# Kernel optimization log

Hardware: AMD Instinct MI355X
Metric: run time of the kernel (lower is better)

The kernel has to match this reference:

```python
import jax, jax.numpy as jnp
import numpy as np
from jax import lax

B, T, D, H, L = 512, 512, 32, 64, 2
ALPHA, BETA = 2.0 / 5.0, 4.0 / 5.0  # GRUFlowBlock contraction constants


def setup_inputs() -> dict:
    key = jax.random.key(0)
    ks = jax.random.split(key, 16)
    s = 1.0 / np.sqrt(H + 1)
    inp = {
        "x": jax.random.normal(ks[0], (B, T, D), jnp.float32),
        "t": jax.random.uniform(ks[1], (B, T, 1), jnp.float32),
        # GRU-flow layer params (spectral norm folded into weight values)
        "flow_W_hr": jax.random.normal(ks[2], (L, H, H + 1), jnp.float32) * s,
        "flow_b_hr": jax.random.normal(ks[3], (L, H), jnp.float32) * 0.01,
        "flow_W_hz": jax.random.normal(ks[4], (L, H, H + 1), jnp.float32) * s,
        "flow_b_hz": jax.random.normal(ks[5], (L, H), jnp.float32) * 0.01,
        "flow_W_hh": jax.random.normal(ks[6], (L, H, H + 1), jnp.float32) * s,
        "flow_b_hh": jax.random.normal(ks[7], (L, H), jnp.float32) * 0.01,
        # TimeTanh: tanh(w * t), per-dim scale w
        "flow_tw": jax.random.normal(ks[8], (L, H), jnp.float32),
        # nn.GRU(D, H) single layer, batch_first
        "gru_W_ih": jax.random.normal(ks[9], (3 * H, D), jnp.float32) / np.sqrt(H),
        "gru_W_hh": jax.random.normal(ks[10], (3 * H, H), jnp.float32) / np.sqrt(H),
        "gru_b_ih": jax.random.normal(ks[11], (3 * H,), jnp.float32) / np.sqrt(H),
        "gru_b_hh": jax.random.normal(ks[12], (3 * H,), jnp.float32) / np.sqrt(H),
    }
    return inp


def _flow(h, tt, flow_W_hr, flow_b_hr, flow_W_hz, flow_b_hz, flow_W_hh, flow_b_hh, flow_tw):
    # h: [B, H], tt: [B, 1]
    for l in range(L):
        inp = jnp.concatenate([h, tt], -1)  # [B, H+1]
        r = BETA * jax.nn.sigmoid(inp @ flow_W_hr[l].T + flow_b_hr[l])
        z = ALPHA * jax.nn.sigmoid(inp @ flow_W_hz[l].T + flow_b_hz[l])
        u = jnp.tanh(jnp.concatenate([r * h, tt], -1) @ flow_W_hh[l].T + flow_b_hh[l])
        h = h + jnp.tanh(flow_tw[l] * tt) * (z * (u - h))
    return h


def _gru_cell(xt, h, gru_W_ih, gru_W_hh, gru_b_ih, gru_b_hh):
    gi = xt @ gru_W_ih.T + gru_b_ih  # [B, 3H]
    gh = h @ gru_W_hh.T + gru_b_hh
    i_r, i_z, i_n = jnp.split(gi, 3, -1)
    h_r, h_z, h_n = jnp.split(gh, 3, -1)
    r = jax.nn.sigmoid(i_r + h_r)
    z = jax.nn.sigmoid(i_z + h_z)
    n = jnp.tanh(i_n + r * h_n)
    return (1.0 - z) * n + z * h


def reference(x, t, flow_W_hr, flow_b_hr, flow_W_hz, flow_b_hz, flow_W_hh, flow_b_hh,
              flow_tw, gru_W_ih, gru_W_hh, gru_b_ih, gru_b_hh):
    def step(h, xt_tt):
        xt, tt = xt_tt  # [B, D], [B, 1]
        h = _flow(h, tt, flow_W_hr, flow_b_hr, flow_W_hz, flow_b_hz,
                  flow_W_hh, flow_b_hh, flow_tw)
        h_out = h  # hiddens stores the post-flow, pre-GRU state
        h_new = _gru_cell(xt, h, gru_W_ih, gru_W_hh, gru_b_ih, gru_b_hh)
        return h_new, h_out

    h0 = jnp.zeros((x.shape[0], H), x.dtype)
    xs = (jnp.swapaxes(x, 0, 1), jnp.swapaxes(t, 0, 1))  # time-major for scan
    _, hiddens = lax.scan(step, h0, xs)  # [T, B, H]
    return jnp.swapaxes(hiddens, 0, 1)  # [B, T, H]
```

## Files before the change

kernel.cpp:

```cpp
#include <hip/hip_runtime.h>


#define NT 512
#define ND 32
#define NH 64
#define NL 2

__device__ __forceinline__ float sigm(float v) {
    return __builtin_amdgcn_rcpf(1.0f + __expf(-v));
}
__device__ __forceinline__ float tanh_(float v) {
    return 1.0f - 2.0f * __builtin_amdgcn_rcpf(1.0f + __expf(2.0f * v));
}

__global__ __launch_bounds__(512, 4) void cgru_fused(
    const float* __restrict__ x, const float* __restrict__ tin,
    const float* __restrict__ Whr, const float* __restrict__ bhr,
    const float* __restrict__ Whz, const float* __restrict__ bhz,
    const float* __restrict__ Whh, const float* __restrict__ bhh,
    const float* __restrict__ tw,
    const float* __restrict__ gWih, const float* __restrict__ gWhh,
    const float* __restrict__ gbih, const float* __restrict__ gbhh,
    float* __restrict__ out)
{
    const int tid = threadIdx.x;
    const int j   = tid >> 3;
    const int q   = tid & 7;
    const int qh  = q & 3;
    const bool isZ = q >= 4;
    const int b   = blockIdx.x;

    __shared__ float hS[NH];
    __shared__ float rhS[NH];
    __shared__ float hxS[128];

    const float* Wsrc = isZ ? Whz : Whr;
    const float* bsrc = isZ ? bhz : bhr;
    float wrz[NL][16], wu[NL][8];
    float w65rz[NL], w65u[NL], brz[NL], bu[NL], tws[NL];
#pragma unroll
    for (int l = 0; l < NL; ++l) {
        const int row = (l * NH + j) * (NH + 1);
#pragma unroll
        for (int k = 0; k < 16; ++k) wrz[l][k] = Wsrc[row + qh * 16 + k];
#pragma unroll
        for (int k = 0; k < 8; ++k)  wu[l][k]  = Whh[row + q * 8 + k];
        w65rz[l] = Wsrc[row + NH];
        w65u[l]  = Whh[row + NH];
        brz[l]   = bsrc[l * NH + j];
        bu[l]    = bhh[l * NH + j];
        tws[l]   = tw[l * NH + j];
    }

    const int grow = (isZ ? NH : 0) + j;
    float g1[24];
#pragma unroll
    for (int k = 0; k < 24; ++k) {
        const int m = qh * 24 + k;
        g1[k] = (m < NH) ? gWhh[grow * NH + m] : gWih[grow * ND + (m - NH)];
    }
    const float bg1 = gbih[grow] + gbhh[grow];

    float g2[16];
    if (!isZ) {
#pragma unroll
        for (int k = 0; k < 16; ++k) g2[k] = gWhh[(2 * NH + j) * NH + qh * 16 + k];
    } else {
#pragma unroll
        for (int k = 0; k < 8; ++k)  g2[k] = gWih[(2 * NH + j) * ND + qh * 8 + k];
#pragma unroll
        for (int k = 8; k < 16; ++k) g2[k] = 0.0f;
    }
    const float bin = gbih[2 * NH + j];
    const float bhn = gbhh[2 * NH + j];

    if (tid < NH) hS[tid] = 0.0f;
    if (tid < 32) hxS[96 + tid] = 0.0f;
    __syncthreads();

    const float* xp = x + (size_t)b * NT * ND;
    const float* tp = tin + (size_t)b * NT;
    float* op = out + (size_t)b * NT * NH;

    for (int ts = 0; ts < NT; ++ts) {
        const float tt = tp[ts];
        float xv = 0.0f;
        if (tid < ND) xv = xp[ts * ND + tid];

#pragma unroll
        for (int l = 0; l < NL; ++l) {
            float a = 0.0f;
            {
                const float* hp = &hS[qh * 16];
#pragma unroll
                for (int k = 0; k < 16; ++k) a = fmaf(wrz[l][k], hp[k], a);
            }
            a += __shfl_xor(a, 1);
            a += __shfl_xor(a, 2);
            const float s  = sigm(a + w65rz[l] * tt + brz[l]);
            const float zv = 0.4f * s;
            if (q == 0) rhS[j] = (0.8f * s) * hS[j];
            __syncthreads();

            float u = 0.0f;
            {
                const float* rp = &rhS[q * 8];
#pragma unroll
                for (int k = 0; k < 8; ++k) u = fmaf(wu[l][k], rp[k], u);
            }
            u += __shfl_xor(u, 1);
            u += __shfl_xor(u, 2);
            u += __shfl_xor(u, 4);
            if (l == NL - 1 && tid < ND) hxS[NH + tid] = xv;
            const float uu = tanh_(u + w65u[l] * tt + bu[l]);
            if (q == 4) {
                const float hj = hS[j];
                const float hn = fmaf(tanh_(tws[l] * tt) * zv, uu - hj, hj);
                hS[j] = hn;
                if (l == NL - 1) {
                    hxS[j] = hn;
                    op[ts * NH + j] = hn;
                }
            }
            __syncthreads();
        }

        float p = 0.0f;
        {
            const float* gp = &hxS[qh * 24];
#pragma unroll
            for (int k = 0; k < 24; ++k) p = fmaf(g1[k], gp[k], p);
        }
        p += __shfl_xor(p, 1);
        p += __shfl_xor(p, 2);
        const float gate = sigm(p + bg1);
        const float oth  = __shfl_xor(gate, 4);
        const float r = isZ ? oth : gate;
        const float z = isZ ? gate : oth;

        float d = 0.0f;
        {
            const float* dp = &hxS[isZ ? (NH + qh * 8) : (qh * 16)];
#pragma unroll
            for (int k = 0; k < 16; ++k) d = fmaf(g2[k], dp[k], d);
        }
        d += __shfl_xor(d, 1);
        d += __shfl_xor(d, 2);
        const float e = __shfl_xor(d, 4);
        const float hnd = isZ ? e : d;
        const float ind = isZ ? d : e;

        const float n  = tanh_(ind + bin + r * (hnd + bhn));
        const float hj = hxS[j];
        const float hp2 = (1.0f - z) * n + z * hj;
        if (q == 0) hS[j] = hp2;
        __syncthreads();
    }
}

extern "C" void kernel_launch(void* const* d_in, const int* in_sizes, int n_in,
                              void* d_out, int out_size, void* d_ws, size_t ws_size,
                              hipStream_t stream) {
    const float* x    = (const float*)d_in[0];
    const float* tin  = (const float*)d_in[1];
    const float* Whr  = (const float*)d_in[2];
    const float* bhr  = (const float*)d_in[3];
    const float* Whz  = (const float*)d_in[4];
    const float* bhz  = (const float*)d_in[5];
    const float* Whh  = (const float*)d_in[6];
    const float* bhh  = (const float*)d_in[7];
    const float* tw   = (const float*)d_in[8];
    const float* gWih = (const float*)d_in[9];
    const float* gWhh = (const float*)d_in[10];
    const float* gbih = (const float*)d_in[11];
    const float* gbhh = (const float*)d_in[12];
    float* out = (float*)d_out;

    dim3 grid(512), block(512);
    hipLaunchKernelGGL(cgru_fused, grid, block, 0, stream,
                       x, tin, Whr, bhr, Whz, bhz, Whh, bhh, tw,
                       gWih, gWhh, gbih, gbhh, out);
}
```

Baseline: 1.385 ms.

## Process two batch rows per block sharing register-resident weights

Each block now runs the recurrence for two independent batch sequences at once, reusing the same per-thread weight registers for both and halving the grid to 256 blocks. Barrier and shuffle latency per timestep is amortised over two sequences, giving more independent work between syncs. It also prefetches the next timestep's x and t values and pins weights in VGPRs with empty asm. The cost is more registers (launch bounds lowered to 2), and with 256 blocks the GPU's 256 CUs each run a single block, which may lower latency hiding.

```diff
diff --git a/kernel.cpp b/kernel.cpp
--- a/kernel.cpp
+++ b/kernel.cpp
@@ -12,8 +12,9 @@
 __device__ __forceinline__ float tanh_(float v) {
     return 1.0f - 2.0f * __builtin_amdgcn_rcpf(1.0f + __expf(2.0f * v));
 }
-
-__global__ __launch_bounds__(512, 4) void cgru_fused(
+#define PIN(v) asm volatile("" : "+v"(v))
+
+__global__ __launch_bounds__(512, 2) void cgru_fused(
     const float* __restrict__ x, const float* __restrict__ tin,
     const float* __restrict__ Whr, const float* __restrict__ bhr,
     const float* __restrict__ Whz, const float* __restrict__ bhz,
@@ -28,11 +29,11 @@
     const int q   = tid & 7;
     const int qh  = q & 3;
     const bool isZ = q >= 4;
-    const int b   = blockIdx.x;
-
-    __shared__ float hS[NH];
-    __shared__ float rhS[NH];
-    __shared__ float hxS[128];
+    const int b0  = blockIdx.x * 2;
+
+    __shared__ float hS[2][NH];
+    __shared__ float rhS[2][NH];
+    __shared__ float hxS[2][128];
 
     const float* Wsrc = isZ ? Whz : Whr;
     const float* bsrc = isZ ? bhz : bhr;
@@ -74,87 +75,154 @@
     const float bin = gbih[2 * NH + j];
     const float bhn = gbhh[2 * NH + j];
 
-    if (tid < NH) hS[tid] = 0.0f;
-    if (tid < 32) hxS[96 + tid] = 0.0f;
+#pragma unroll
+    for (int l = 0; l < NL; ++l) {
+#pragma unroll
+        for (int k = 0; k < 16; ++k) PIN(wrz[l][k]);
+#pragma unroll
+        for (int k = 0; k < 8; ++k)  PIN(wu[l][k]);
+        PIN(w65rz[l]); PIN(w65u[l]); PIN(brz[l]); PIN(bu[l]); PIN(tws[l]);
+    }
+#pragma unroll
+    for (int k = 0; k < 24; ++k) PIN(g1[k]);
+#pragma unroll
+    for (int k = 0; k < 16; ++k) PIN(g2[k]);
+    float bg1p = bg1, binp = bin, bhnp = bhn;
+    PIN(bg1p); PIN(binp); PIN(bhnp);
+
+    if (tid < 2 * NH) ((float*)hS)[tid] = 0.0f;
+    if (tid < 2 * ND) hxS[tid >> 5][96 + (tid & 31)] = 0.0f;
     __syncthreads();
 
-    const float* xp = x + (size_t)b * NT * ND;
-    const float* tp = tin + (size_t)b * NT;
-    float* op = out + (size_t)b * NT * NH;
+    const float* xptr = x + (size_t)(b0 + (tid >= ND ? 1 : 0)) * NT * ND;
+    const float* tp0  = tin + (size_t)b0 * NT;
+    const float* tp1  = tin + (size_t)(b0 + 1) * NT;
+    float* op0 = out + (size_t)b0 * NT * NH;
+    float* op1 = out + (size_t)(b0 + 1) * NT * NH;
+
+    float xv = 0.0f;
+    if (tid < 2 * ND) xv = xptr[tid & 31];
+    float tt0 = tp0[0], tt1 = tp1[0];
 
     for (int ts = 0; ts < NT; ++ts) {
-        const float tt = tp[ts];
-        float xv = 0.0f;
-        if (tid < ND) xv = xp[ts * ND + tid];
+        float xnext = 0.0f, ttn0 = 0.0f, ttn1 = 0.0f;
+        if (ts + 1 < NT) {
+            if (tid < 2 * ND) xnext = xptr[(ts + 1) * ND + (tid & 31)];
+            ttn0 = tp0[ts + 1];
+            ttn1 = tp1[ts + 1];
+        }
 
 #pragma unroll
         for (int l = 0; l < NL; ++l) {
-            float a = 0.0f;
+            float a0 = 0.0f, a1 = 0.0f;
             {
-                const float* hp = &hS[qh * 16];
-#pragma unroll
-                for (int k = 0; k < 16; ++k) a = fmaf(wrz[l][k], hp[k], a);
-            }
-            a += __shfl_xor(a, 1);
-            a += __shfl_xor(a, 2);
-            const float s  = sigm(a + w65rz[l] * tt + brz[l]);
-            const float zv = 0.4f * s;
-            if (q == 0) rhS[j] = (0.8f * s) * hS[j];
+                const float* hp0 = &hS[0][qh * 16];
+                const float* hp1 = &hS[1][qh * 16];
+#pragma unroll
+                for (int k = 0; k < 16; ++k) {
+                    a0 = fmaf(wrz[l][k], hp0[k], a0);
+                    a1 = fmaf(wrz[l][k], hp1[k], a1);
+                }
+            }
+            a0 += __shfl_xor(a0, 1); a0 += __shfl_xor(a0, 2);
+            a1 += __shfl_xor(a1, 1); a1 += __shfl_xor(a1, 2);
+            const float s0 = sigm(a0 + w65rz[l] * tt0 + brz[l]);
+            const float s1 = sigm(a1 + w65rz[l] * tt1 + brz[l]);
+            const float zv0 = 0.4f * s0;
+            const float zv1 = 0.4f * s1;
+            if (q == 0) {
+                rhS[0][j] = (0.8f * s0) * hS[0][j];
+                rhS[1][j] = (0.8f * s1) * hS[1][j];
+            }
             __syncthreads();
 
-            float u = 0.0f;
+            float u0 = 0.0f, u1 = 0.0f;
             {
-                const float* rp = &rhS[q * 8];
-#pragma unroll
-                for (int k = 0; k < 8; ++k) u = fmaf(wu[l][k], rp[k], u);
-            }
-            u += __shfl_xor(u, 1);
-            u += __shfl_xor(u, 2);
-            u += __shfl_xor(u, 4);
-            if (l == NL - 1 && tid < ND) hxS[NH + tid] = xv;
-            const float uu = tanh_(u + w65u[l] * tt + bu[l]);
+                const float* rp0 = &rhS[0][q * 8];
+                const float* rp1 = &rhS[1][q * 8];
+#pragma unroll
+                for (int k = 0; k < 8; ++k) {
+                    u0 = fmaf(wu[l][k], rp0[k], u0);
+                    u1 = fmaf(wu[l][k], rp1[k], u1);
+                }
+            }
+            u0 += __shfl_xor(u0, 1); u0 += __shfl_xor(u0, 2); u0 += __shfl_xor(u0, 4);
+            u1 += __shfl_xor(u1, 1); u1 += __shfl_xor(u1, 2); u1 += __shfl_xor(u1, 4);
+            if (l == NL - 1 && tid < 2 * ND)
+                hxS[tid >> 5][NH + (tid & 31)] = xv;
+            const float uu0 = tanh_(u0 + w65u[l] * tt0 + bu[l]);
+            const float uu1 = tanh_(u1 + w65u[l] * tt1 + bu[l]);
             if (q == 4) {
-                const float hj = hS[j];
-                const float hn = fmaf(tanh_(tws[l] * tt) * zv, uu - hj, hj);
-                hS[j] = hn;
+                const float h0 = hS[0][j];
+                const float h1 = hS[1][j];
+                const float hn0 = fmaf(tanh_(tws[l] * tt0) * zv0, uu0 - h0, h0);
+                const float hn1 = fmaf(tanh_(tws[l] * tt1) * zv1, uu1 - h1, h1);
+                hS[0][j] = hn0;
+                hS[1][j] = hn1;
                 if (l == NL - 1) {
-                    hxS[j] = hn;
-                    op[ts * NH + j] = hn;
+                    hxS[0][j] = hn0;
+                    hxS[1][j] = hn1;
+                    op0[ts * NH + j] = hn0;
+                    op1[ts * NH + j] = hn1;
                 }
             }
             __syncthreads();
         }
 
-        float p = 0.0f;
+        float p0 = 0.0f, p1 = 0.0f;
         {
-            const float* gp = &hxS[qh * 24];
-#pragma unroll
-            for (int k = 0; k < 24; ++k) p = fmaf(g1[k], gp[k], p);
-        }
-        p += __shfl_xor(p, 1);
-        p += __shfl_xor(p, 2);
-        const float gate = sigm(p + bg1);
-        const float oth  = __shfl_xor(gate, 4);
-        const float r = isZ ? oth : gate;
-        const float z = isZ ? gate : oth;
-
-        float d = 0.0f;
+            const float* gp0 = &hxS[0][qh * 24];
+            const float* gp1 = &hxS[1][qh * 24];
+#pragma unroll
+            for (int k = 0; k < 24; ++k) {
+                p0 = fmaf(g1[k], gp0[k], p0);
+                p1 = fmaf(g1[k], gp1[k], p1);
+            }
+        }
+        p0 += __shfl_xor(p0, 1); p0 += __shfl_xor(p0, 2);
+        p1 += __shfl_xor(p1, 1); p1 += __shfl_xor(p1, 2);
+        const float gate0 = sigm(p0 + bg1p);
+        const float gate1 = sigm(p1 + bg1p);
+        const float oth0  = __shfl_xor(gate0, 4);
+        const float oth1  = __shfl_xor(gate1, 4);
+        const float r0 = isZ ? oth0 : gate0;
+        const float r1 = isZ ? oth1 : gate1;
+        const float z0 = isZ ? gate0 : oth0;
+        const float z1 = isZ ? gate1 : oth1;
+
+        float d0 = 0.0f, d1 = 0.0f;
         {
-            const float* dp = &hxS[isZ ? (NH + qh * 8) : (qh * 16)];
-#pragma unroll
-            for (int k = 0; k < 16; ++k) d = fmaf(g2[k], dp[k], d);
-        }
-        d += __shfl_xor(d, 1);
-        d += __shfl_xor(d, 2);
-        const float e = __shfl_xor(d, 4);
-        const float hnd = isZ ? e : d;
-        const float ind = isZ ? d : e;
-
-        const float n  = tanh_(ind + bin + r * (hnd + bhn));
-        const float hj = hxS[j];
-        const float hp2 = (1.0f - z) * n + z * hj;
-        if (q == 0) hS[j] = hp2;
+            const int off = isZ ? (NH + qh * 8) : (qh * 16);
+            const float* dp0 = &hxS[0][off];
+            const float* dp1 = &hxS[1][off];
+#pragma unroll
+            for (int k = 0; k < 16; ++k) {
+                d0 = fmaf(g2[k], dp0[k], d0);
+                d1 = fmaf(g2[k], dp1[k], d1);
+            }
+        }
+        d0 += __shfl_xor(d0, 1); d0 += __shfl_xor(d0, 2);
+        d1 += __shfl_xor(d1, 1); d1 += __shfl_xor(d1, 2);
+        const float e0 = __shfl_xor(d0, 4);
+        const float e1 = __shfl_xor(d1, 4);
+        const float hnd0 = isZ ? e0 : d0;
+        const float hnd1 = isZ ? e1 : d1;
+        const float ind0 = isZ ? d0 : e0;
+        const float ind1 = isZ ? d1 : e1;
+
+        const float n0 = tanh_(ind0 + binp + r0 * (hnd0 + bhnp));
+        const float n1 = tanh_(ind1 + binp + r1 * (hnd1 + bhnp));
+        const float hj0 = hxS[0][j];
+        const float hj1 = hxS[1][j];
+        const float hp20 = (1.0f - z0) * n0 + z0 * hj0;
+        const float hp21 = (1.0f - z1) * n1 + z1 * hj1;
+        if (q == 0) {
+            hS[0][j] = hp20;
+            hS[1][j] = hp21;
+        }
         __syncthreads();
+
+        xv = xnext; tt0 = ttn0; tt1 = ttn1;
     }
 }
 
@@ -176,7 +244,7 @@
     const float* gbhh = (const float*)d_in[12];
     float* out = (float*)d_out;
 
-    dim3 grid(512), block(512);
+    dim3 grid(256), block(512);
     hipLaunchKernelGGL(cgru_fused, grid, block, 0, stream,
                        x, tin, Whr, bhr, Whz, bhz, Whh, bhh, tw,
                        gWih, gWhh, gbih, gbhh, out);
```

Result: no change. 1.383 ms (-0.1%).
